# Optimization experiments

Hardware: AMD Instinct MI355X
Metric: run time of the kernel (lower is better)

## Reference

```python
import jax, jax.numpy as jnp
import numpy as np

B, T, D = 2, 2048, 2048
H, KV, HD, RD = 16, 4, 128, 64  # n_heads, n_kv_heads, head_dim, rope_head_dim
THETA = 10000.0


def setup_inputs() -> dict:
    key = jax.random.key(0)
    ks = jax.random.split(key, 5)
    x = jax.random.normal(ks[0], (B, T, D), dtype=jnp.float32)
    Wq = jax.random.normal(ks[1], (D, H * HD), dtype=jnp.float32) * 0.02
    Wk = jax.random.normal(ks[2], (D, KV * HD), dtype=jnp.float32) * 0.02
    Wv = jax.random.normal(ks[3], (D, KV * HD), dtype=jnp.float32) * 0.02
    Wo = jax.random.normal(ks[4], (H * HD, D), dtype=jnp.float32) * 0.02
    # RoPE frequencies for the first RD dims of each head
    inv_freq = 1.0 / (THETA ** (jnp.arange(0, RD, 2, dtype=jnp.float32) / RD))  # [RD/2]
    ang = jnp.arange(T, dtype=jnp.float32)[:, None] * inv_freq[None, :]         # [T, RD/2]
    return {"x": x, "freqs_cos": jnp.cos(ang), "freqs_sin": jnp.sin(ang),
            "Wq": Wq, "Wk": Wk, "Wv": Wv, "Wo": Wo}


def _apply_rope(t, cos, sin):
    # t: [B, h, T, HD]; rotate first RD dims treating consecutive pairs as complex
    rot = t[..., :RD].reshape(*t.shape[:-1], RD // 2, 2)
    e, o = rot[..., 0], rot[..., 1]
    c = cos[None, None]  # [1,1,T,RD/2]
    s = sin[None, None]
    re = e * c - o * s
    ro = e * s + o * c
    rot_out = jnp.stack([re, ro], axis=-1).reshape(*t.shape[:-1], RD)
    return jnp.concatenate([rot_out, t[..., RD:]], axis=-1)


def reference(x, freqs_cos, freqs_sin, Wq, Wk, Wv, Wo):
    q = (x @ Wq).reshape(B, T, H, HD).transpose(0, 2, 1, 3)   # [B,H,T,HD]
    k = (x @ Wk).reshape(B, T, KV, HD).transpose(0, 2, 1, 3)  # [B,KV,T,HD]
    v = (x @ Wv).reshape(B, T, KV, HD).transpose(0, 2, 1, 3)
    q = _apply_rope(q, freqs_cos, freqs_sin)
    k = _apply_rope(k, freqs_cos, freqs_sin)
    present_k, present_v = k, v
    rep = H // KV
    kr = jnp.repeat(k, rep, axis=1)  # GQA repeat_interleave -> [B,H,T,HD]
    vr = jnp.repeat(v, rep, axis=1)
    scores = jnp.einsum('bhqd,bhkd->bhqk', q, kr) / jnp.sqrt(jnp.asarray(HD, q.dtype))
    causal = jnp.tril(jnp.ones((T, T), dtype=bool))
    scores = jnp.where(causal[None, None], scores, jnp.asarray(-1e9, scores.dtype))
    attn = jax.nn.softmax(scores, axis=-1)
    y = jnp.einsum('bhqk,bhkd->bhqd', attn, vr)
    y = y.transpose(0, 2, 1, 3).reshape(B, T, H * HD) @ Wo  # [B,T,D]
    return y, present_k, present_v
```

## Files before the change

### kernel.cpp

```cpp
#include <hip/hip_runtime.h>
#include <hip/hip_bf16.h>

static constexpr int B_  = 2;
static constexpr int T_  = 2048;
static constexpr int D_  = 2048;
static constexpr int H_  = 16;
static constexpr int KV_ = 4;
static constexpr int HD_ = 128;
static constexpr int RD_ = 64;
static constexpr int BT_ = B_ * T_;
static constexpr int NPROJ_ = 3072;
static constexpr float SCALE_ = 0.08838834764831845f;

typedef __attribute__((ext_vector_type(8))) short bf16x8;
typedef __attribute__((ext_vector_type(8))) unsigned short u16x8;
typedef __attribute__((ext_vector_type(4))) float f32x4;

#define COMPILER_BARRIER() __asm__ __volatile__("" ::: "memory")
#define BAR() do { COMPILER_BARRIER(); __builtin_amdgcn_s_barrier(); COMPILER_BARRIER(); } while (0)

typedef const __attribute__((address_space(1))) unsigned int* as1_u32p;
typedef __attribute__((address_space(3))) unsigned int* as3_u32p;
#define GLOAD16(g, l) __builtin_amdgcn_global_load_lds((as1_u32p)(const void*)(g), (as3_u32p)(void*)(l), 16, 0, 0)

__device__ __forceinline__ unsigned short f2bu(float f) {
  unsigned x = __float_as_uint(f);
  unsigned r = (x + 0x7fffu + ((x >> 16) & 1u)) >> 16;
  return (unsigned short)r;
}

__global__ __launch_bounds__(256) void cvt_bf16(const float* __restrict__ in,
                                                unsigned short* __restrict__ out) {
  const size_t i = ((size_t)blockIdx.x * 256 + threadIdx.x) * 4;
  const float4 f = *(const float4*)(in + i);
  ushort4 o;
  o.x = f2bu(f.x); o.y = f2bu(f.y); o.z = f2bu(f.z); o.w = f2bu(f.w);
  *(ushort4*)(out + i) = o;
}

__global__ __launch_bounds__(256) void t32_all(const float* __restrict__ Wq,
                                               const float* __restrict__ Wk,
                                               const float* __restrict__ Wv,
                                               const float* __restrict__ Wo,
                                               unsigned short* __restrict__ Wqt,
                                               unsigned short* __restrict__ Wkvt,
                                               unsigned short* __restrict__ Wot) {
  const float* in; unsigned short* out; int C;
  switch (blockIdx.z) {
    case 0:  in = Wq; out = Wqt;                       C = 2048; break;
    case 1:  in = Wk; out = Wkvt;                      C = 512;  break;
    case 2:  in = Wv; out = Wkvt + (size_t)512 * D_;   C = 512;  break;
    default: in = Wo; out = Wot;                       C = 2048; break;
  }
  if ((int)blockIdx.y * 32 >= C) return;

  __shared__ unsigned short tile[32][36];
  const int r0 = blockIdx.x * 32;
  const int c0 = blockIdx.y * 32;
  const int tid = threadIdx.x;
  {
    const int r = tid >> 3;
    const int c = (tid & 7) * 4;
    const float4 f = *(const float4*)(in + (size_t)(r0 + r) * C + c0 + c);
    ushort4 w;
    w.x = f2bu(f.x); w.y = f2bu(f.y); w.z = f2bu(f.z); w.w = f2bu(f.w);
    *(ushort4*)&tile[r][c] = w;
  }
  __syncthreads();
  {
    const int c = tid >> 3;
    const int r = (tid & 7) * 4;
    ushort4 o;
    o.x = tile[r + 0][c];
    o.y = tile[r + 1][c];
    o.z = tile[r + 2][c];
    o.w = tile[r + 3][c];
    *(ushort4*)(out + (size_t)(c0 + c) * D_ + r0 + r) = o;
  }
}

template <int EPI>
__global__ __launch_bounds__(512, 1) void gemm256(const unsigned short* __restrict__ A,
                                                  const unsigned short* __restrict__ Bt,
                                                  float* __restrict__ C,
                                                  unsigned short* __restrict__ Qbf,
                                                  float* __restrict__ kout,
                                                  float* __restrict__ vout,
                                                  unsigned short* __restrict__ Kbf,
                                                  const float* __restrict__ cosb,
                                                  const float* __restrict__ sinb,
                                                  int N) {
  __shared__ __align__(16) unsigned short As[2][256 * 64];
  __shared__ __align__(16) unsigned short Bs[2][256 * 64];
  constexpr int K = D_;
  constexpr int KT = K / 64;

  const int tid = threadIdx.x;
  const int lane = tid & 63;
  const int wave = tid >> 6;
  const int n16 = lane & 15;
  const int quad = lane >> 4;
  const int wm = wave >> 2;
  const int wn = wave & 3;

  const int nwg = gridDim.x * gridDim.y;
  int bid = blockIdx.y * gridDim.x + blockIdx.x;
  bid = (bid & 7) * (nwg >> 3) + (bid >> 3);
  const int bn = (bid % (int)gridDim.x) * 256;
  const int bm = (bid / (int)gridDim.x) * 256;

  const int t8 = tid >> 3;
  const int kg = ((tid & 7) ^ (t8 & 7)) << 3;
  const unsigned short *aS0[2], *aS1[2], *bS0[2], *bS1[2];
#pragma unroll
  for (int g = 0; g < 2; ++g) {
    aS0[g] = A + (size_t)(bm + g * 128 + t8) * K + kg;
    aS1[g] = A + (size_t)(bm + g * 128 + 64 + t8) * K + kg;
    const int br = (g * 2 + (t8 >> 5)) * 64 + (t8 & 31);
    bS0[g] = Bt + (size_t)(bn + br) * K + kg;
    bS1[g] = Bt + (size_t)(bn + br + 32) * K + kg;
  }

#define STAGE(dst, half, src, koff)                                             \
  do {                                                                          \
    GLOAD16((src)[0] + (koff), &(dst)[((half) * 128 + 0) * 64 + wave * 512]);   \
    GLOAD16((src)[1] + (koff), &(dst)[((half) * 128 + 64) * 64 + wave * 512]);  \
  } while (0)

#define LDA(MH)                                                                   \
  _Pragma("unroll") for (int ks = 0; ks < 2; ++ks)                                \
  _Pragma("unroll") for (int i = 0; i < 4; ++i)                                   \
      aF[ks][i] = *(const bf16x8*)&cA[((MH) * 128 + wm * 64 + i * 16 + n16) * 64  \
                                      + ((quad * 8 + ks * 32) ^ ((n16 & 7) << 3))];

#define LDB(DST, NH)                                                              \
  _Pragma("unroll") for (int ks = 0; ks < 2; ++ks)                                \
  _Pragma("unroll") for (int jj = 0; jj < 2; ++jj)                                \
      DST[ks][jj] = *(const bf16x8*)&cB[((NH) * 128 + wn * 32 + jj * 16 + n16) * 64 \
                                        + ((quad * 8 + ks * 32) ^ ((n16 & 7) << 3))];

#define MFQ(MH, NH, BF)                                                           \
  do {                                                                            \
    __builtin_amdgcn_s_setprio(1);                                                \
    _Pragma("unroll") for (int ks = 0; ks < 2; ++ks)                              \
    _Pragma("unroll") for (int i = 0; i < 4; ++i)                                 \
    _Pragma("unroll") for (int jj = 0; jj < 2; ++jj)                              \
        acc[(MH) * 4 + i][(NH) * 2 + jj] = __builtin_amdgcn_mfma_f32_16x16x32_bf16( \
            aF[ks][i], BF[ks][jj], acc[(MH) * 4 + i][(NH) * 2 + jj], 0, 0, 0);    \
    __builtin_amdgcn_s_setprio(0);                                                \
  } while (0)

  f32x4 acc[8][4];
#pragma unroll
  for (int mi = 0; mi < 8; ++mi)
#pragma unroll
    for (int ni = 0; ni < 4; ++ni) acc[mi][ni] = (f32x4){0.f, 0.f, 0.f, 0.f};

  bf16x8 aF[2][4], b0F[2][2], b1F[2][2];

  STAGE(As[0], 0, aS0, 0);
  STAGE(Bs[0], 0, bS0, 0);
  STAGE(Bs[0], 1, bS1, 0);
  STAGE(As[0], 1, aS1, 0);

  for (int kt = 0; kt < KT - 1; ++kt) {
    const unsigned short* cA = As[kt & 1];
    const unsigned short* cB = Bs[kt & 1];
    unsigned short* nA = As[(kt & 1) ^ 1];
    unsigned short* nB = Bs[(kt & 1) ^ 1];
    const int ko = (kt + 1) * 64;

    STAGE(nA, 0, aS0, ko);
    asm volatile("s_waitcnt vmcnt(6)" ::: "memory");
    BAR();
    LDA(0); LDB(b0F, 0);
    MFQ(0, 0, b0F);
    STAGE(nB, 0, bS0, ko);
    asm volatile("s_waitcnt vmcnt(6)" ::: "memory");
    BAR();
    LDB(b1F, 1);
    MFQ(0, 1, b1F);
    STAGE(nB, 1, bS1, ko);
    asm volatile("s_waitcnt vmcnt(6)" ::: "memory");
    BAR();
    LDA(1);
    MFQ(1, 0, b0F);
    STAGE(nA, 1, aS1, ko);
    MFQ(1, 1, b1F);
  }

  {
    const unsigned short* cA = As[(KT - 1) & 1];
    const unsigned short* cB = Bs[(KT - 1) & 1];
    asm volatile("s_waitcnt vmcnt(4)" ::: "memory");
    BAR();
    LDA(0); LDB(b0F, 0);
    MFQ(0, 0, b0F);
    asm volatile("s_waitcnt vmcnt(2)" ::: "memory");
    BAR();
    LDB(b1F, 1);
    MFQ(0, 1, b1F);
    asm volatile("s_waitcnt vmcnt(0)" ::: "memory");
    BAR();
    LDA(1);
    MFQ(1, 0, b0F);
    MFQ(1, 1, b1F);
  }

#pragma unroll
  for (int mi = 0; mi < 8; ++mi) {
#pragma unroll
    for (int rr = 0; rr < 4; ++rr) {
      const int row = bm + wm * 128 + mi * 16 + quad * 4 + rr;
      if (EPI == 0) {
#pragma unroll
        for (int ni = 0; ni < 4; ++ni) {
          const int col = bn + wn * 64 + ni * 16 + n16;
          C[(size_t)row * N + col] = acc[mi][ni][rr];
        }
      } else {
        const int b = row >> 11, t = row & (T_ - 1);
#pragma unroll
        for (int ni = 0; ni < 4; ++ni) {
          const int col = bn + wn * 64 + ni * 16 + n16;
          const int hd = col & 127;
          float v = acc[mi][ni][rr];
          const float other = __shfl_xor(v, 1);
          if (col < 2560 && hd < RD_) {
            const float c = cosb[t * 32 + (hd >> 1)];
            const float s = sinb[t * 32 + (hd >> 1)];
            v = (col & 1) ? (other * s + v * c) : (v * c - other * s);
          }
          if (col < 2048) {
            Qbf[(size_t)row * (H_ * HD_) + col] = f2bu(v * SCALE_);
          } else if (col < 2560) {
            const int kv = (col - 2048) >> 7;
            const size_t idx = (((size_t)(b * KV_ + kv) * T_) + t) * HD_ + hd;
            kout[idx] = v;
            Kbf[idx] = f2bu(v);
          } else {
            const int kv = (col - 2560) >> 7;
            vout[(((size_t)(b * KV_ + kv) * T_) + t) * HD_ + hd] = v;
          }
        }
      }
    }
  }
#undef STAGE
#undef LDA
#undef LDB
#undef MFQ
}

__global__ __launch_bounds__(256) void v_transpose(const float* __restrict__ vin,
                                                   unsigned short* __restrict__ vt) {
  __shared__ unsigned int tile[32][17];
  const int tid = threadIdx.x;
  const int k0 = blockIdx.x * 32;
  const int d0 = blockIdx.y * 32;
  const int g  = blockIdx.z;
  const float* src = vin + ((size_t)g * T_ + k0) * HD_ + d0;

  {
    const int kr = tid >> 3;
    const int d2 = (tid & 7) * 2;
#pragma unroll
    for (int c = 0; c < 2; ++c) {
      const float2 f = *(const float2*)(src + (size_t)kr * HD_ + (d2 + c) * 2);
      tile[kr][d2 + c] = (unsigned)f2bu(f.x) | ((unsigned)f2bu(f.y) << 16);
    }
  }
  __syncthreads();
  {
    const int dr = tid >> 3;
    const int kc = (tid & 7) * 4;
    const int dstb = ((kc & 15) << 1) | ((kc & 16) >> 2);
    const int hi = dr >> 1;
    const int sh = (dr & 1) * 16;
    ushort4 o;
    o.x = (unsigned short)(tile[kc + 0][hi] >> sh);
    o.y = (unsigned short)(tile[kc + 1][hi] >> sh);
    o.z = (unsigned short)(tile[kc + 2][hi] >> sh);
    o.w = (unsigned short)(tile[kc + 3][hi] >> sh);
    *(ushort4*)(vt + ((size_t)g * HD_ + d0 + dr) * T_ + k0 + dstb) = o;
  }
}

__global__ __launch_bounds__(256, 2) void attn_flash(const unsigned short* __restrict__ Q,
                                                     const unsigned short* __restrict__ Kbf,
                                                     const unsigned short* __restrict__ VbfT,
                                                     unsigned short* __restrict__ O) {
  __shared__ __align__(16) unsigned short Ks[32 * 128];
  __shared__ __align__(16) unsigned short Vs[128 * 32];

  const int tid = threadIdx.x;
  const int wave = tid >> 6;
  const int lane = tid & 63;
  const int n16 = lane & 15;
  const int quad = lane >> 4;
  const int pid = blockIdx.x;
  const int q0A = pid * 16;
  const int q0B = (127 - pid) * 16;
  const int nchA = (q0A + 47) >> 5;
  const int nchB = (q0B + 47) >> 5;
  const int bkv = blockIdx.y;
  const int b = bkv >> 2;
  const int kvh = bkv & 3;
  const int h = kvh * 4 + wave;

  const unsigned short* ksrc = Kbf + ((size_t)(b * KV_ + kvh)) * T_ * HD_;
  const unsigned short* vtsrc = VbfT + ((size_t)(b * KV_ + kvh)) * HD_ * T_;

  const int krow = tid >> 4;
  const int kcol = (tid & 15) * 8;
  const int kdst0 = (krow * 128 + kcol) ^ ((krow & 7) << 3);
  const int kdst1 = ((krow + 16) * 128 + kcol) ^ ((krow & 7) << 3);
  const int vrow = tid >> 2;
  const int vcol = (tid & 3) * 8;
  const int vdst0 = (vrow * 32 + vcol) ^ ((vrow & 3) << 3);
  const int vdst1 = ((vrow + 64) * 32 + vcol) ^ ((vrow & 3) << 3);

  bf16x8 qfA[4], qfB[4];
  {
    const unsigned short* qa = Q + ((size_t)(b * T_ + q0A + n16)) * (H_ * HD_) + h * HD_ + quad * 8;
    const unsigned short* qb = Q + ((size_t)(b * T_ + q0B + n16)) * (H_ * HD_) + h * HD_ + quad * 8;
#pragma unroll
    for (int s = 0; s < 4; ++s) {
      qfA[s] = *(const bf16x8*)(qa + s * 32);
      qfB[s] = *(const bf16x8*)(qb + s * 32);
    }
  }

  float mA = -1e30f, lA = 0.f;
  float mB = -1e30f, lB = 0.f;
  f32x4 oA[8], oB[8];
#pragma unroll
  for (int t = 0; t < 8; ++t) { oA[t] = (f32x4){0.f,0.f,0.f,0.f}; oB[t] = (f32x4){0.f,0.f,0.f,0.f}; }

  {
    const u16x8 ka = *(const u16x8*)(ksrc + (size_t)krow * HD_ + kcol);
    const u16x8 kb = *(const u16x8*)(ksrc + (size_t)(krow + 16) * HD_ + kcol);
    const u16x8 va = *(const u16x8*)(vtsrc + (size_t)vrow * T_ + vcol);
    const u16x8 vb = *(const u16x8*)(vtsrc + (size_t)(vrow + 64) * T_ + vcol);
    *(u16x8*)&Ks[kdst0] = ka;
    *(u16x8*)&Ks[kdst1] = kb;
    *(u16x8*)&Vs[vdst0] = va;
    *(u16x8*)&Vs[vdst1] = vb;
  }
  __syncthreads();

  for (int c = 0; c < nchB; ++c) {
    const int kc = c * 32;
    const bool actA = (c < nchA);

    u16x8 ka, kb, va, vb;
    if (c + 1 < nchB) {
      ka = *(const u16x8*)(ksrc + (size_t)(kc + 32 + krow) * HD_ + kcol);
      kb = *(const u16x8*)(ksrc + (size_t)(kc + 48 + krow) * HD_ + kcol);
      va = *(const u16x8*)(vtsrc + (size_t)vrow * T_ + (kc + 32) + vcol);
      vb = *(const u16x8*)(vtsrc + (size_t)(vrow + 64) * T_ + (kc + 32) + vcol);
    }
    COMPILER_BARRIER();

    f32x4 sB0 = (f32x4){0.f,0.f,0.f,0.f}, sB1 = sB0, sA0 = sB0, sA1 = sB0;
#pragma unroll
    for (int s = 0; s < 4; ++s) {
      const bf16x8 kf0 = *(const bf16x8*)&Ks[(n16 * 128 + quad * 8 + s * 32) ^ ((n16 & 7) << 3)];
      const bf16x8 kf1 = *(const bf16x8*)&Ks[((16 + n16) * 128 + quad * 8 + s * 32) ^ ((n16 & 7) << 3)];
      sB0 = __builtin_amdgcn_mfma_f32_16x16x32_bf16(kf0, qfB[s], sB0, 0, 0, 0);
      sB1 = __builtin_amdgcn_mfma_f32_16x16x32_bf16(kf1, qfB[s], sB1, 0, 0, 0);
      if (actA) {
        sA0 = __builtin_amdgcn_mfma_f32_16x16x32_bf16(kf0, qfA[s], sA0, 0, 0, 0);
        sA1 = __builtin_amdgcn_mfma_f32_16x16x32_bf16(kf1, qfA[s], sA1, 0, 0, 0);
      }
    }

    union { bf16x8 v; unsigned short u[8]; } pkB, pkA;
    bool growB;
    float alphaB = 1.f, alphaA = 1.f;
    {
      float s[8];
#pragma unroll
      for (int r = 0; r < 4; ++r) { s[r] = sB0[r]; s[r + 4] = sB1[r]; }
      if (c == nchB - 1) {
        const int qrow = q0B + n16;
#pragma unroll
        for (int r = 0; r < 4; ++r) {
          if (kc + quad * 4 + r > qrow)      s[r]     = -1e30f;
          if (kc + 16 + quad * 4 + r > qrow) s[r + 4] = -1e30f;
        }
      }
      float mm = fmaxf(fmaxf(fmaxf(s[0], s[1]), fmaxf(s[2], s[3])),
                       fmaxf(fmaxf(s[4], s[5]), fmaxf(s[6], s[7])));
      mm = fmaxf(mm, __shfl_xor(mm, 16));
      mm = fmaxf(mm, __shfl_xor(mm, 32));
      growB = __any(mm > mB);
      if (growB) {
        const float mnew = fmaxf(mB, mm);
        alphaB = __expf(mB - mnew);
        mB = mnew;
      }
      float lsum = 0.f;
#pragma unroll
      for (int j = 0; j < 8; ++j) {
        const float p = __expf(s[j] - mB);
        lsum += p;
        pkB.u[j] = f2bu(p);
      }
      lsum += __shfl_xor(lsum, 16);
      lsum += __shfl_xor(lsum, 32);
      lB = growB ? (alphaB * lB + lsum) : (lB + lsum);
    }

    bool growA = false;
    if (actA) {
      float s[8];
#pragma unroll
      for (int r = 0; r < 4; ++r) { s[r] = sA0[r]; s[r + 4] = sA1[r]; }
      if (c == nchA - 1) {
        const int qrow = q0A + n16;
#pragma unroll
        for (int r = 0; r < 4; ++r) {
          if (kc + quad * 4 + r > qrow)      s[r]     = -1e30f;
          if (kc + 16 + quad * 4 + r > qrow) s[r + 4] = -1e30f;
        }
      }
      float mm = fmaxf(fmaxf(fmaxf(s[0], s[1]), fmaxf(s[2], s[3])),
                       fmaxf(fmaxf(s[4], s[5]), fmaxf(s[6], s[7])));
      mm = fmaxf(mm, __shfl_xor(mm, 16));
      mm = fmaxf(mm, __shfl_xor(mm, 32));
      growA = __any(mm > mA);
      if (growA) {
        const float mnew = fmaxf(mA, mm);
        alphaA = __expf(mA - mnew);
        mA = mnew;
      }
      float lsum = 0.f;
#pragma unroll
      for (int j = 0; j < 8; ++j) {
        const float p = __expf(s[j] - mA);
        lsum += p;
        pkA.u[j] = f2bu(p);
      }
      lsum += __shfl_xor(lsum, 16);
      lsum += __shfl_xor(lsum, 32);
      lA = growA ? (alphaA * lA + lsum) : (lA + lsum);
    }

    if (growB) {
      f32x4 av;
#pragma unroll
      for (int r = 0; r < 4; ++r) av[r] = __shfl(alphaB, quad * 4 + r);
#pragma unroll
      for (int t = 0; t < 8; ++t) {
        oB[t][0] *= av[0]; oB[t][1] *= av[1]; oB[t][2] *= av[2]; oB[t][3] *= av[3];
      }
    }
    if (growA) {
      f32x4 av;
#pragma unroll
      for (int r = 0; r < 4; ++r) av[r] = __shfl(alphaA, quad * 4 + r);
#pragma unroll
      for (int t = 0; t < 8; ++t) {
        oA[t][0] *= av[0]; oA[t][1] *= av[1]; oA[t][2] *= av[2]; oA[t][3] *= av[3];
      }
    }

#pragma unroll
    for (int t = 0; t < 8; ++t) {
      const bf16x8 vf = *(const bf16x8*)&Vs[((t * 16 + n16) * 32 + quad * 8) ^ ((n16 & 3) << 3)];
      oB[t] = __builtin_amdgcn_mfma_f32_16x16x32_bf16(pkB.v, vf, oB[t], 0, 0, 0);
      if (actA) oA[t] = __builtin_amdgcn_mfma_f32_16x16x32_bf16(pkA.v, vf, oA[t], 0, 0, 0);
    }

    __syncthreads();
    if (c + 1 < nchB) {
      *(u16x8*)&Ks[kdst0] = ka;
      *(u16x8*)&Ks[kdst1] = kb;
      *(u16x8*)&Vs[vdst0] = va;
      *(u16x8*)&Vs[vdst1] = vb;
    }
    __syncthreads();
  }

  {
    unsigned short* obB = O + ((size_t)(b * T_ + q0B)) * (H_ * HD_) + h * HD_;
    unsigned short* obA = O + ((size_t)(b * T_ + q0A)) * (H_ * HD_) + h * HD_;
#pragma unroll
    for (int r = 0; r < 4; ++r) {
      const float liB = 1.0f / __shfl(lB, quad * 4 + r);
      const float liA = 1.0f / __shfl(lA, quad * 4 + r);
#pragma unroll
      for (int t = 0; t < 8; ++t) {
        obB[(size_t)(quad * 4 + r) * (H_ * HD_) + t * 16 + n16] = f2bu(oB[t][r] * liB);
        obA[(size_t)(quad * 4 + r) * (H_ * HD_) + t * 16 + n16] = f2bu(oA[t][r] * liA);
      }
    }
  }
}

extern "C" void kernel_launch(void* const* d_in, const int* in_sizes, int n_in,
                              void* d_out, int out_size, void* d_ws, size_t ws_size,
                              hipStream_t stream) {
  const float* x  = (const float*)d_in[0];
  const float* fc = (const float*)d_in[1];
  const float* fs = (const float*)d_in[2];
  const float* Wq = (const float*)d_in[3];
  const float* Wk = (const float*)d_in[4];
  const float* Wv = (const float*)d_in[5];
  const float* Wo = (const float*)d_in[6];

  float* yout = (float*)d_out;
  float* kout = yout + (size_t)B_ * T_ * D_;
  float* vout = kout + (size_t)B_ * KV_ * T_ * HD_;
  unsigned short* Qbf = (unsigned short*)yout;

  unsigned short* xb   = (unsigned short*)d_ws;
  unsigned short* Abf  = xb;
  unsigned short* Wqt  = xb   + (size_t)BT_ * D_;
  unsigned short* Wkvt = Wqt  + (size_t)D_ * D_;
  unsigned short* Wot  = Wkvt + (size_t)1024 * D_;
  unsigned short* Kbf  = Wot  + (size_t)D_ * D_;
  unsigned short* VbfT = Kbf  + (size_t)B_ * KV_ * T_ * HD_;

  dim3 blk(256);

  cvt_bf16<<<dim3((BT_ * D_) / 1024), blk, 0, stream>>>(x, xb);
  t32_all<<<dim3(D_ / 32, D_ / 32, 4), blk, 0, stream>>>(Wq, Wk, Wv, Wo, Wqt, Wkvt, Wot);

  gemm256<1><<<dim3(NPROJ_ / 256, BT_ / 256), dim3(512), 0, stream>>>(
      xb, Wqt, nullptr, Qbf, kout, vout, Kbf, fc, fs, NPROJ_);

  v_transpose<<<dim3(T_ / 32, HD_ / 32, B_ * KV_), blk, 0, stream>>>(vout, VbfT);

  attn_flash<<<dim3(64, B_ * KV_), blk, 0, stream>>>(Qbf, Kbf, VbfT, Abf);

  gemm256<0><<<dim3(D_ / 256, BT_ / 256), dim3(512), 0, stream>>>(
      Abf, Wot, yout, nullptr, nullptr, nullptr, nullptr, nullptr, nullptr, D_);
}
```

Baseline: 379.9 us.

## Issue all next-tile loads upfront and cut per-iteration barriers in projection GEMM

The projection GEMM main loop now issues all four global-to-LDS stages for the next k-tile at the start of each iteration, waits once, and synchronises with two barriers instead of interleaving stages with three wait/barrier pairs. A second A-fragment register set (aG) lets both A halves be held at once, and the MFMA quadrants are reordered to reuse B fragments. The aim is fewer barriers and a simpler schedule, at the cost of more VGPRs and less fine-grained overlap of loads with compute. The wait count vmcnt(8) assumes the four new stages leave exactly eight loads outstanding, meaning the previous tile has fully landed.

Measured after the change: 386.2 us. Within noise of the previous version (+1.7%).

```diff
diff --git a/kernel.cpp b/kernel.cpp
--- a/kernel.cpp
+++ b/kernel.cpp
@@ -127,26 +127,26 @@
     GLOAD16((src)[1] + (koff), &(dst)[((half) * 128 + 64) * 64 + wave * 512]);  \
   } while (0)
 
-#define LDA(MH)                                                                   \
+#define LDA_(DST, MH)                                                             \
   _Pragma("unroll") for (int ks = 0; ks < 2; ++ks)                                \
   _Pragma("unroll") for (int i = 0; i < 4; ++i)                                   \
-      aF[ks][i] = *(const bf16x8*)&cA[((MH) * 128 + wm * 64 + i * 16 + n16) * 64  \
-                                      + ((quad * 8 + ks * 32) ^ ((n16 & 7) << 3))];
-
-#define LDB(DST, NH)                                                              \
+      DST[ks][i] = *(const bf16x8*)&cA[((MH) * 128 + wm * 64 + i * 16 + n16) * 64 \
+                                       + ((quad * 8 + ks * 32) ^ ((n16 & 7) << 3))];
+
+#define LDB_(DST, NH)                                                             \
   _Pragma("unroll") for (int ks = 0; ks < 2; ++ks)                                \
   _Pragma("unroll") for (int jj = 0; jj < 2; ++jj)                                \
       DST[ks][jj] = *(const bf16x8*)&cB[((NH) * 128 + wn * 32 + jj * 16 + n16) * 64 \
                                         + ((quad * 8 + ks * 32) ^ ((n16 & 7) << 3))];
 
-#define MFQ(MH, NH, BF)                                                           \
+#define MFQ(MH, NH, AF, BF)                                                       \
   do {                                                                            \
     __builtin_amdgcn_s_setprio(1);                                                \
     _Pragma("unroll") for (int ks = 0; ks < 2; ++ks)                              \
     _Pragma("unroll") for (int i = 0; i < 4; ++i)                                 \
     _Pragma("unroll") for (int jj = 0; jj < 2; ++jj)                              \
         acc[(MH) * 4 + i][(NH) * 2 + jj] = __builtin_amdgcn_mfma_f32_16x16x32_bf16( \
-            aF[ks][i], BF[ks][jj], acc[(MH) * 4 + i][(NH) * 2 + jj], 0, 0, 0);    \
+            AF[ks][i], BF[ks][jj], acc[(MH) * 4 + i][(NH) * 2 + jj], 0, 0, 0);    \
     __builtin_amdgcn_s_setprio(0);                                                \
   } while (0)
 
@@ -156,7 +156,7 @@
 #pragma unroll
     for (int ni = 0; ni < 4; ++ni) acc[mi][ni] = (f32x4){0.f, 0.f, 0.f, 0.f};
 
-  bf16x8 aF[2][4], b0F[2][2], b1F[2][2];
+  bf16x8 aF[2][4], aG[2][4], b0F[2][2], b1F[2][2];
 
   STAGE(As[0], 0, aS0, 0);
   STAGE(Bs[0], 0, bS0, 0);
@@ -171,40 +171,37 @@
     const int ko = (kt + 1) * 64;
 
     STAGE(nA, 0, aS0, ko);
-    asm volatile("s_waitcnt vmcnt(6)" ::: "memory");
+    STAGE(nB, 0, bS0, ko);
+    STAGE(nB, 1, bS1, ko);
+    STAGE(nA, 1, aS1, ko);
+    asm volatile("s_waitcnt vmcnt(8)" ::: "memory");
     BAR();
-    LDA(0); LDB(b0F, 0);
-    MFQ(0, 0, b0F);
-    STAGE(nB, 0, bS0, ko);
-    asm volatile("s_waitcnt vmcnt(6)" ::: "memory");
+
+    LDA_(aF, 0);
+    LDB_(b0F, 0);
+    LDB_(b1F, 1);
+    MFQ(0, 0, aF, b0F);
+    LDA_(aG, 1);
+    MFQ(0, 1, aF, b1F);
+    MFQ(1, 1, aG, b1F);
+    MFQ(1, 0, aG, b0F);
+
     BAR();
-    LDB(b1F, 1);
-    MFQ(0, 1, b1F);
-    STAGE(nB, 1, bS1, ko);
-    asm volatile("s_waitcnt vmcnt(6)" ::: "memory");
-    BAR();
-    LDA(1);
-    MFQ(1, 0, b0F);
-    STAGE(nA, 1, aS1, ko);
-    MFQ(1, 1, b1F);
   }
 
   {
     const unsigned short* cA = As[(KT - 1) & 1];
     const unsigned short* cB = Bs[(KT - 1) & 1];
-    asm volatile("s_waitcnt vmcnt(4)" ::: "memory");
-    BAR();
-    LDA(0); LDB(b0F, 0);
-    MFQ(0, 0, b0F);
-    asm volatile("s_waitcnt vmcnt(2)" ::: "memory");
-    BAR();
-    LDB(b1F, 1);
-    MFQ(0, 1, b1F);
     asm volatile("s_waitcnt vmcnt(0)" ::: "memory");
     BAR();
-    LDA(1);
-    MFQ(1, 0, b0F);
-    MFQ(1, 1, b1F);
+    LDA_(aF, 0);
+    LDB_(b0F, 0);
+    LDB_(b1F, 1);
+    MFQ(0, 0, aF, b0F);
+    LDA_(aG, 1);
+    MFQ(0, 1, aF, b1F);
+    MFQ(1, 1, aG, b1F);
+    MFQ(1, 0, aG, b0F);
   }
 
 #pragma unroll
@@ -247,8 +244,8 @@
     }
   }
 #undef STAGE
-#undef LDA
-#undef LDB
+#undef LDA_
+#undef LDB_
 #undef MFQ
 }
 
```
